# Kernel tuning notes

Measured on AMD Instinct MI355X. Metric: run time of the kernel, lower is better.

The kernel has to match this reference:

```python
import jax, jax.numpy as jnp
import numpy as np

EPS = 1e-8
SQRT_EPS_LOSS = 1e-6


def setup_inputs() -> dict:
    key = jax.random.key(0)
    ks = jax.random.split(key, 8)
    n_vars, n_clauses, n_edges, n_graphs = 500_000, 2_000_000, 6_000_000, 256
    dim, k = 128, 8
    x = jax.random.normal(ks[0], (n_vars, dim), jnp.float32)
    polarity = jnp.where(jax.random.bernoulli(ks[1], 0.5, (n_edges,)), 1.0, -1.0).astype(jnp.float32)
    variable_indices = jax.random.randint(ks[2], (n_edges,), 0, n_vars)
    clause_indices = jax.random.randint(ks[3], (n_edges,), 0, n_clauses)
    clause_batch = jnp.sort(jax.random.randint(ks[4], (n_clauses,), 0, n_graphs))
    W1 = jax.random.normal(ks[5], (dim, dim), jnp.float32) / np.sqrt(dim).astype(np.float32)
    b1 = jnp.zeros((dim,), jnp.float32)
    W2 = jax.random.normal(ks[6], (dim, k), jnp.float32) / np.sqrt(dim).astype(np.float32)
    b2 = jnp.zeros((k,), jnp.float32)
    return dict(x=x, polarity=polarity, variable_indices=variable_indices,
                clause_indices=clause_indices, clause_batch=clause_batch,
                W1=W1, b1=b1, W2=W2, b2=b2, n_graphs=n_graphs)


def reference(x, polarity, variable_indices, clause_indices, clause_batch, W1, b1, W2, b2, n_graphs):
    n_clauses = clause_batch.shape[0]
    k = W2.shape[1]

    # variables_output MLP: Linear -> ReLU -> Linear, [n_vars, k]
    logits = jax.nn.relu(x @ W1 + b1) @ W2 + b2

    # softplus_mixed_loss: gather literals along edges, scatter-sum into clauses
    lit = logits[variable_indices] * polarity[:, None]                      # [E, k]
    clause_sum = jax.ops.segment_sum(jax.nn.softplus(lit), clause_indices,
                                     num_segments=n_clauses)                # [C, k]
    clause_val = jnp.exp(-clause_sum)
    per_clause_loss = clause_val * (-jnp.log(1.0 - clause_val + EPS))       # [C, k]

    # per-graph soft loss
    per_graph_loss = jax.ops.segment_sum(per_clause_loss, clause_batch,
                                         num_segments=n_graphs)             # [G, k]
    per_graph_loss = jnp.sqrt(per_graph_loss + SQRT_EPS_LOSS) - np.float32(np.sqrt(SQRT_EPS_LOSS))

    costs = jnp.square(jnp.arange(1, k + 1, dtype=jnp.float32))             # [k]
    sorted_desc = -jnp.sort(-per_graph_loss, axis=-1)                       # descending sort per graph
    logit_loss = jnp.sum(sorted_desc * costs) / jnp.sum(costs)              # scalar

    # hard assignment check
    logits_hard = jnp.where(logits > 0, 1.0, -1.0)
    edge_hard = logits_hard[variable_indices] * polarity[:, None]           # [E, k]
    clauses_hard = jax.ops.segment_max(edge_hard, clause_indices,
                                       num_segments=n_clauses)              # amax per clause
    graphs_hard = jax.ops.segment_min(clauses_hard, clause_batch,
                                      num_segments=n_graphs)                # amin per graph
    solved = jnp.any(graphs_hard > 0.5, axis=1)                             # [G] bool

    return logit_loss, solved
```

## Files before the change

kernel.cpp:

```cpp
#include <hip/hip_runtime.h>
#include <hip/hip_bf16.h>

#define DIM 128
#define K 8
#define EPS 1e-8f
#define SQRT_EPS 1e-6f

#define CB 512
#define CSHIFT 9
#define NBMAX 4096
#define MAXSLOT 32
#define SARR_CAP 2560

#define TV1 8192
#define NT1MAX 1024
#define NKV 512
#define VSH 10
#define TB 4096
#define MAXTV 4
#define NKC 64
#define TC 4096
#define MAXTC 32

typedef __attribute__((ext_vector_type(8))) short bf16x8;
typedef __attribute__((ext_vector_type(4))) float f32x4;

__device__ inline short bfc(float f) {
    union { __hip_bfloat16 h; short s; } u;
    u.h = __float2bfloat16(f);
    return u.s;
}

#define LDW 136

__global__ __launch_bounds__(256) void mlp_kernel(
    const float* __restrict__ x, const float* __restrict__ W1,
    const float* __restrict__ b1, const float* __restrict__ W2,
    const float* __restrict__ b2, uint2* __restrict__ lfp8, int n_vars)
{
    __shared__ __align__(16) short w1t[DIM][LDW];
    __shared__ __align__(16) short w2t[16][LDW];
    __shared__ __align__(16) short hlds[4][16][LDW];
    __shared__ __align__(16) float lout[4][32][8];

    const int t = threadIdx.x;
    const int wave = t >> 6, lane = t & 63;
    const int lr = lane & 15, lg = lane >> 4;

    for (int i = t; i < DIM * DIM; i += 256) {
        int r = i >> 7, c = i & 127;
        w1t[c][r] = bfc(W1[i]);
    }
    for (int i = t; i < 16 * DIM; i += 256) {
        int c = i >> 7, j = i & 127;
        w2t[c][j] = (c < 8) ? bfc(W2[j * 8 + c]) : (short)0;
    }
    __syncthreads();

    const int rbase = blockIdx.x * 128 + wave * 32;

    bf16x8 a[2][4];
    #pragma unroll
    for (int rt = 0; rt < 2; ++rt) {
        int row = rbase + rt * 16 + lr;
        bool ok = row < n_vars;
        const float* xp = x + (size_t)row * DIM + lg * 8;
        #pragma unroll
        for (int kt = 0; kt < 4; ++kt) {
            bf16x8 av = {0,0,0,0,0,0,0,0};
            if (ok) {
                float4 f0 = *(const float4*)(xp + kt * 32);
                float4 f1 = *(const float4*)(xp + kt * 32 + 4);
                av[0]=bfc(f0.x); av[1]=bfc(f0.y); av[2]=bfc(f0.z); av[3]=bfc(f0.w);
                av[4]=bfc(f1.x); av[5]=bfc(f1.y); av[6]=bfc(f1.z); av[7]=bfc(f1.w);
            }
            a[rt][kt] = av;
        }
    }

    bf16x8 bb[4];
    #pragma unroll
    for (int kt = 0; kt < 4; ++kt)
        bb[kt] = *(const bf16x8*)&w2t[lr][kt * 32 + lg * 8];
    float b2v = (lr < 8) ? b2[lr] : 0.f;

    #pragma unroll
    for (int rt = 0; rt < 2; ++rt) {
        #pragma unroll
        for (int n = 0; n < 8; ++n) {
            f32x4 acc = {0.f, 0.f, 0.f, 0.f};
            #pragma unroll
            for (int kt = 0; kt < 4; ++kt) {
                bf16x8 bf = *(const bf16x8*)&w1t[n * 16 + lr][kt * 32 + lg * 8];
                acc = __builtin_amdgcn_mfma_f32_16x16x32_bf16(a[rt][kt], bf, acc, 0, 0, 0);
            }
            float bcol = b1[n * 16 + lr];
            #pragma unroll
            for (int r = 0; r < 4; ++r) {
                float h = fmaxf(acc[r] + bcol, 0.f);
                hlds[wave][lg * 4 + r][n * 16 + lr] = bfc(h);
            }
        }
        f32x4 acc2 = {0.f, 0.f, 0.f, 0.f};
        #pragma unroll
        for (int kt = 0; kt < 4; ++kt) {
            bf16x8 af = *(const bf16x8*)&hlds[wave][lr][kt * 32 + lg * 8];
            acc2 = __builtin_amdgcn_mfma_f32_16x16x32_bf16(af, bb[kt], acc2, 0, 0, 0);
        }
        if (lr < 8) {
            #pragma unroll
            for (int r = 0; r < 4; ++r)
                lout[wave][rt * 16 + lg * 4 + r][lr] = acc2[r] + b2v;
        }
    }

    __syncthreads();
    if (lane < 32) {
        int row = rbase + lane;
        if (row < n_vars) {
            const float* f = lout[wave][lane];
            unsigned lo = 0u, hi = 0u;
            lo = __builtin_amdgcn_cvt_pk_fp8_f32(f[0], f[1], lo, false);
            lo = __builtin_amdgcn_cvt_pk_fp8_f32(f[2], f[3], lo, true);
            hi = __builtin_amdgcn_cvt_pk_fp8_f32(f[4], f[5], hi, false);
            hi = __builtin_amdgcn_cvt_pk_fp8_f32(f[6], f[7], hi, true);
            lfp8[row] = make_uint2(lo, hi);
        }
    }
}


__global__ __launch_bounds__(256) void histV_kernel(
    const int* __restrict__ vi, unsigned* __restrict__ histV, int n_edges)
{
    __shared__ unsigned hl[NKV];
    const int t = threadIdx.x, b = blockIdx.x;
    for (int i = t; i < NKV; i += 256) hl[i] = 0u;
    __syncthreads();
    const int e0 = b * TV1, e1 = min(e0 + TV1, n_edges);
    for (int e = e0 + t; e < e1; e += 256)
        atomicAdd(&hl[((unsigned)vi[e]) >> VSH], 1u);
    __syncthreads();
    for (int i = t; i < NKV; i += 256) histV[(size_t)i * NT1MAX + b] = hl[i];
}

__global__ __launch_bounds__(256) void scanrowV_kernel(
    unsigned* __restrict__ hist, unsigned* __restrict__ btotal)
{
    const int t = threadIdx.x;
    const size_t base = (size_t)blockIdx.x * NT1MAX + t * 4;
    uint4 v = *(const uint4*)(hist + base);
    unsigned pre0 = 0, pre1 = v.x, pre2 = v.x + v.y, pre3 = v.x + v.y + v.z;
    unsigned run = pre3 + v.w;
    __shared__ unsigned ts[256];
    ts[t] = run;
    __syncthreads();
    for (int off = 1; off < 256; off <<= 1) {
        unsigned xv = (t >= off) ? ts[t - off] : 0u;
        __syncthreads();
        ts[t] += xv;
        __syncthreads();
    }
    unsigned ex = ts[t] - run;
    uint4 o = {ex + pre0, ex + pre1, ex + pre2, ex + pre3};
    *(uint4*)(hist + base) = o;
    if (t == 255) btotal[blockIdx.x] = ts[255];
}

__global__ void baseV_kernel(const unsigned* __restrict__ tv,
                             unsigned* __restrict__ bv)
{
    if (threadIdx.x == 0) {
        unsigned r = 0;
        for (int k = 0; k < NKV; ++k) { bv[k] = r; r += tv[k]; }
        bv[NKV] = r;
    }
}

__global__ __launch_bounds__(256) void scatterV_kernel(
    const int* __restrict__ ci, const int* __restrict__ vi,
    const float* __restrict__ pol, const unsigned* __restrict__ histV,
    const unsigned* __restrict__ baseV, unsigned* __restrict__ A, int n_edges)
{
    __shared__ unsigned sa[TV1];
    __shared__ unsigned short bmap[TV1];
    __shared__ unsigned h[NKV], lst[NKV], h2[NKV], gst[NKV];
    __shared__ unsigned ts[256];
    const int t = threadIdx.x, b = blockIdx.x;
    for (int i = t; i < NKV; i += 256) h[i] = 0u;
    __syncthreads();
    const int e0 = b * TV1, e1 = min(e0 + TV1, n_edges), n = e1 - e0;
    for (int e = e0 + t; e < e1; e += 256)
        atomicAdd(&h[((unsigned)vi[e]) >> VSH], 1u);
    __syncthreads();
    unsigned a0 = h[2 * t], a1 = h[2 * t + 1];
    unsigned run = a0 + a1;
    ts[t] = run;
    __syncthreads();
    for (int off = 1; off < 256; off <<= 1) {
        unsigned xv = (t >= off) ? ts[t - off] : 0u;
        __syncthreads();
        ts[t] += xv;
        __syncthreads();
    }
    unsigned ex = ts[t] - run;
    lst[2 * t] = ex; lst[2 * t + 1] = ex + a0;
    h2[2 * t] = ex;  h2[2 * t + 1] = ex + a0;
    __syncthreads();
    for (int e = e0 + t; e < e1; e += 256) {
        unsigned c = (unsigned)ci[e];
        unsigned v = (unsigned)vi[e];
        unsigned neg = (pol[e] < 0.f) ? 1u : 0u;
        unsigned k = v >> VSH;
        unsigned p = atomicAdd(&h2[k], 1u);
        sa[p] = c | (neg << 21) | ((v & ((1u << VSH) - 1u)) << 22);
        bmap[p] = (unsigned short)k;
    }
    for (int i = t; i < NKV; i += 256)
        gst[i] = baseV[i] + histV[(size_t)i * NT1MAX + b];
    __syncthreads();
    for (int s = t; s < n; s += 256) {
        unsigned k = bmap[s];
        A[gst[k] + (s - lst[k])] = sa[s];
    }
}


__global__ __launch_bounds__(256) void histB_kernel(
    const unsigned* __restrict__ A, const unsigned* __restrict__ baseV,
    unsigned* __restrict__ histB)
{
    __shared__ unsigned h[NKC];
    const int t = threadIdx.x;
    const int vg = blockIdx.x / MAXTV, i = blockIdx.x % MAXTV;
    const unsigned slo = baseV[vg], shi = baseV[vg + 1];
    const unsigned t0 = slo + (unsigned)i * TB;
    if (t0 >= shi) return;
    const unsigned t1 = min(t0 + TB, shi);
    if (t < NKC) h[t] = 0u;
    __syncthreads();
    for (unsigned e = t0 + t; e < t1; e += 256)
        atomicAdd(&h[(A[e] & 0x1FFFFFu) >> 15], 1u);
    __syncthreads();
    if (t < NKC) histB[(size_t)t * (NKV * MAXTV) + blockIdx.x] = h[t];
}

__global__ __launch_bounds__(256) void scanrowB_kernel(
    unsigned* __restrict__ hist, unsigned* __restrict__ btotal)
{
    const int t = threadIdx.x;
    const size_t base = (size_t)blockIdx.x * (NKV * MAXTV) + t * 8;
    uint4 v0 = *(const uint4*)(hist + base);
    uint4 v1 = *(const uint4*)(hist + base + 4);
    unsigned p0 = 0, p1 = v0.x, p2 = p1 + v0.y, p3 = p2 + v0.z, p4 = p3 + v0.w;
    unsigned p5 = p4 + v1.x, p6 = p5 + v1.y, p7 = p6 + v1.z;
    unsigned run = p7 + v1.w;
    __shared__ unsigned ts[256];
    ts[t] = run;
    __syncthreads();
    for (int off = 1; off < 256; off <<= 1) {
        unsigned xv = (t >= off) ? ts[t - off] : 0u;
        __syncthreads();
        ts[t] += xv;
        __syncthreads();
    }
    unsigned ex = ts[t] - run;
    uint4 o0 = {ex + p0, ex + p1, ex + p2, ex + p3};
    uint4 o1 = {ex + p4, ex + p5, ex + p6, ex + p7};
    *(uint4*)(hist + base) = o0;
    *(uint4*)(hist + base + 4) = o1;
    if (t == 255) btotal[blockIdx.x] = ts[255];
}

__global__ void baseB_kernel(const unsigned* __restrict__ tb,
                             unsigned* __restrict__ bb)
{
    if (threadIdx.x == 0) {
        unsigned r = 0;
        for (int k = 0; k < NKC; ++k) { bb[k] = r; r += tb[k]; }
        bb[NKC] = r;
    }
}

__global__ __launch_bounds__(256) void scatterB_kernel(
    const unsigned* __restrict__ A, const uint2* __restrict__ lfp8,
    const unsigned* __restrict__ baseV, const unsigned* __restrict__ histB,
    const unsigned* __restrict__ baseB, unsigned short* __restrict__ B1,
    uint2* __restrict__ B2, int n_vars)
{
    __shared__ uint2 slice[1 << VSH];
    __shared__ unsigned short st1[TB];
    __shared__ uint2 st2[TB];
    __shared__ unsigned char bmap[TB];
    __shared__ unsigned h[NKC], lst[NKC], h2[NKC], gst[NKC];
    const int t = threadIdx.x;
    const int vg = blockIdx.x / MAXTV, i = blockIdx.x % MAXTV;
    const unsigned slo = baseV[vg], shi = baseV[vg + 1];
    const unsigned t0 = slo + (unsigned)i * TB;
    if (t0 >= shi) return;
    const unsigned t1 = min(t0 + TB, shi);
    const int n = (int)(t1 - t0);
    for (int s = t; s < (1 << VSH); s += 256) {
        int v = (vg << VSH) + s;
        slice[s] = (v < n_vars) ? lfp8[v] : make_uint2(0u, 0u);
    }
    if (t < NKC) h[t] = 0u;
    __syncthreads();
    for (unsigned e = t0 + t; e < t1; e += 256)
        atomicAdd(&h[(A[e] & 0x1FFFFFu) >> 15], 1u);
    __syncthreads();
    if (t == 0) {
        unsigned r = 0;
        for (int k = 0; k < NKC; ++k) { lst[k] = r; h2[k] = r; r += h[k]; }
    }
    __syncthreads();
    for (unsigned e = t0 + t; e < t1; e += 256) {
        unsigned a = A[e];
        unsigned c = a & 0x1FFFFFu;
        unsigned k = c >> 15;
        unsigned p = atomicAdd(&h2[k], 1u);
        uint2 g = slice[a >> 22];
        unsigned sm = ((a >> 21) & 1u) * 0x80808080u;
        g.x ^= sm; g.y ^= sm;
        st1[p] = (unsigned short)(c & 0x7FFFu);
        st2[p] = g;
        bmap[p] = (unsigned char)k;
    }
    if (t < NKC) gst[t] = baseB[t] + histB[(size_t)t * (NKV * MAXTV) + blockIdx.x];
    __syncthreads();
    for (int s = t; s < n; s += 256) {
        unsigned k = bmap[s];
        unsigned pos = gst[k] + (s - lst[k]);
        B1[pos] = st1[s];
        B2[pos] = st2[s];
    }
}


__global__ __launch_bounds__(256) void histC_kernel(
    const unsigned short* __restrict__ B1, const unsigned* __restrict__ baseB,
    unsigned* __restrict__ histC)
{
    __shared__ unsigned h[64];
    const int t = threadIdx.x;
    const int k1 = blockIdx.x / MAXTC, i = blockIdx.x % MAXTC;
    const unsigned slo = baseB[k1], shi = baseB[k1 + 1];
    const unsigned t0 = slo + (unsigned)i * TC;
    if (t0 >= shi) return;
    const unsigned t1 = min(t0 + TC, shi);
    if (t < 64) h[t] = 0u;
    __syncthreads();
    for (unsigned e = t0 + t; e < t1; e += 256)
        atomicAdd(&h[((unsigned)B1[e] >> 9) & 63u], 1u);
    __syncthreads();
    if (t < 64) histC[(size_t)(k1 * 64 + t) * MAXTC + i] = h[t];
}

__global__ __launch_bounds__(256) void scanrowC_kernel(
    unsigned* __restrict__ histC, unsigned* __restrict__ ctotal)
{
    const int rid = blockIdx.x * 256 + threadIdx.x;
    unsigned r = 0;
    for (int i = 0; i < MAXTC; ++i) {
        unsigned v = histC[(size_t)rid * MAXTC + i];
        histC[(size_t)rid * MAXTC + i] = r;
        r += v;
    }
    ctotal[rid] = r;
}

__global__ __launch_bounds__(256) void bbase_kernel(
    const unsigned* __restrict__ ctotal, unsigned* __restrict__ bbase, int nb)
{
    const int t = threadIdx.x;
    unsigned loc[16];
    unsigned run = 0;
    #pragma unroll
    for (int it = 0; it < 16; ++it) {
        int idx = t * 16 + it;
        unsigned v = (idx < 4096) ? ctotal[idx] : 0u;
        loc[it] = run;
        run += v;
    }
    __shared__ unsigned ts[256];
    ts[t] = run;
    __syncthreads();
    for (int off = 1; off < 256; off <<= 1) {
        unsigned xv = (t >= off) ? ts[t - off] : 0u;
        __syncthreads();
        ts[t] += xv;
        __syncthreads();
    }
    unsigned ex = ts[t] - run;
    #pragma unroll
    for (int it = 0; it < 16; ++it) {
        int idx = t * 16 + it;
        if (idx <= nb) bbase[idx] = ex + loc[it];
    }
}

__global__ __launch_bounds__(256) void scatterC_kernel(
    const unsigned short* __restrict__ B1, const uint2* __restrict__ B2,
    const unsigned* __restrict__ baseB, const unsigned* __restrict__ histC,
    const unsigned* __restrict__ bbase, unsigned short* __restrict__ sortedS,
    uint2* __restrict__ sortedL)
{
    __shared__ unsigned short st1[TC];
    __shared__ uint2 st2[TC];
    __shared__ unsigned char bmap[TC];
    __shared__ unsigned h[64], lst[64], h2[64], gst[64];
    const int t = threadIdx.x;
    const int k1 = blockIdx.x / MAXTC, i = blockIdx.x % MAXTC;
    const unsigned slo = baseB[k1], shi = baseB[k1 + 1];
    const unsigned t0 = slo + (unsigned)i * TC;
    if (t0 >= shi) return;
    const unsigned t1 = min(t0 + TC, shi);
    const int n = (int)(t1 - t0);
    if (t < 64) h[t] = 0u;
    __syncthreads();
    for (unsigned e = t0 + t; e < t1; e += 256)
        atomicAdd(&h[((unsigned)B1[e] >> 9) & 63u], 1u);
    __syncthreads();
    if (t == 0) {
        unsigned r = 0;
        for (int k = 0; k < 64; ++k) { lst[k] = r; h2[k] = r; r += h[k]; }
    }
    __syncthreads();
    for (unsigned e = t0 + t; e < t1; e += 256) {
        unsigned b = (unsigned)B1[e];
        unsigned k2 = (b >> 9) & 63u;
        unsigned p = atomicAdd(&h2[k2], 1u);
        st1[p] = (unsigned short)(b & 0x1FFu);
        st2[p] = B2[e];
        bmap[p] = (unsigned char)k2;
    }
    if (t < 64) {
        unsigned cbk = (unsigned)(k1 * 64 + t);
        gst[t] = bbase[cbk] + histC[(size_t)cbk * MAXTC + i];
    }
    __syncthreads();
    for (int s = t; s < n; s += 256) {
        unsigned k = bmap[s];
        unsigned pos = gst[k] + (s - lst[k]);
        sortedS[pos] = st1[s];
        sortedL[pos] = st2[s];
    }
}

__global__ __launch_bounds__(256) void bucket_kernel(
    const unsigned short* __restrict__ sortedS, const uint2* __restrict__ sortedL,
    const unsigned* __restrict__ bbase, const int* __restrict__ clause_batch,
    float* __restrict__ per_graph, unsigned* __restrict__ gmask,
    int n_clauses, int n_graphs)
{
    __shared__ uint2 sarrL[SARR_CAP];
    __shared__ unsigned cnt[CB];
    __shared__ unsigned cofs[CB];
    __shared__ unsigned cst[CB + 1];
    __shared__ unsigned cmsk[CB];
    __shared__ float pcl[CB * K];
    __shared__ float sp[256];
    __shared__ float pg[MAXSLOT * K];
    __shared__ unsigned pmask[MAXSLOT];
    __shared__ unsigned ts[256];
    __shared__ int sh_ghi;

    const int t = threadIdx.x;
    const int bkt = blockIdx.x;
    const int c_base = bkt << CSHIFT;
    const int n_cl = min(CB, n_clauses - c_base);
    const int g_lo = clause_batch[c_base];

    {
        float v = __builtin_amdgcn_cvt_f32_fp8((unsigned)t, 0);
        sp[t] = fmaxf(v, 0.f) + __logf(1.f + __expf(-fabsf(v)));
    }
    for (int i = t; i < CB; i += 256) cnt[i] = 0u;
    for (int i = t; i < MAXSLOT * K; i += 256) pg[i] = 0.f;
    if (t < MAXSLOT) pmask[t] = 0xFFu;
    if (t == 0) sh_ghi = clause_batch[c_base + n_cl - 1];
    __syncthreads();

    const unsigned lo = bbase[bkt], hi = bbase[bkt + 1];
    const int ne = (int)(hi - lo);

    if (ne <= SARR_CAP) {
        for (unsigned e = lo + t; e < hi; e += 256)
            atomicAdd(&cnt[sortedS[e] & 511u], 1u);
        __syncthreads();
        unsigned a0 = cnt[2 * t], a1 = cnt[2 * t + 1];
        unsigned run = a0 + a1;
        ts[t] = run;
        __syncthreads();
        for (int off = 1; off < 256; off <<= 1) {
            unsigned xv = (t >= off) ? ts[t - off] : 0u;
            __syncthreads();
            ts[t] += xv;
            __syncthreads();
        }
        unsigned ex = ts[t] - run;
        cst[2 * t] = ex; cst[2 * t + 1] = ex + a0;
        cofs[2 * t] = ex; cofs[2 * t + 1] = ex + a0;
        if (t == 255) cst[CB] = ex + run;
        __syncthreads();
        for (unsigned e = lo + t; e < hi; e += 256) {
            unsigned cl = sortedS[e] & 511u;
            unsigned p = atomicAdd(&cofs[cl], 1u);
            sarrL[p] = sortedL[e];
        }
        __syncthreads();
        #pragma unroll
        for (int oc = 0; oc < 2; ++oc) {
            int cl = 2 * t + oc;
            if (cl >= n_cl) continue;
            unsigned s0 = cst[cl];
            int n = (int)(cst[cl + 1] - s0);
            float sums[K] = {0.f, 0.f, 0.f, 0.f, 0.f, 0.f, 0.f, 0.f};
            unsigned ormask = 0u;
            for (int base = 0; base < n; base += 8) {
                int m = min(8, n - base);
                uint2 gs[8];
                for (int i2 = 0; i2 < m; ++i2) gs[i2] = sarrL[s0 + base + i2];
                for (int i2 = 0; i2 < m; ++i2) {
                    #pragma unroll
                    for (int j = 0; j < 4; ++j) {
                        unsigned b0 = (gs[i2].x >> (8 * j)) & 0xFFu;
                        unsigned b1 = (gs[i2].y >> (8 * j)) & 0xFFu;
                        sums[j]     += sp[b0];
                        sums[j + 4] += sp[b1];
                        ormask |= (b0 - 1u < 0x7Fu) ? (1u << j) : 0u;
                        ormask |= (b1 - 1u < 0x7Fu) ? (1u << (j + 4)) : 0u;
                    }
                }
            }
            #pragma unroll
            for (int j = 0; j < K; ++j) {
                float cv = __expf(-sums[j]);
                pcl[cl * K + j] = cv * (-__logf(1.f - cv + EPS));
            }
            cmsk[cl] = ormask;
        }
    } else {
        for (int i = t; i < CB * K; i += 256) pcl[i] = 0.f;
        for (int i = t; i < CB; i += 256) cmsk[i] = 0u;
        __syncthreads();
        for (unsigned e = lo + t; e < hi; e += 256) {
            unsigned cl = sortedS[e] & 511u;
            uint2 g = sortedL[e];
            unsigned gt0 = 0u;
            #pragma unroll
            for (int j = 0; j < 4; ++j) {
                unsigned b0 = (g.x >> (8 * j)) & 0xFFu;
                unsigned b1 = (g.y >> (8 * j)) & 0xFFu;
                atomicAdd(&pcl[cl * K + j], sp[b0]);
                atomicAdd(&pcl[cl * K + j + 4], sp[b1]);
                gt0 |= (b0 - 1u < 0x7Fu) ? (1u << j) : 0u;
                gt0 |= (b1 - 1u < 0x7Fu) ? (1u << (j + 4)) : 0u;
            }
            atomicOr(&cmsk[cl], gt0);
        }
        __syncthreads();
        for (int oc = 0; oc < 2; ++oc) {
            int cl = 2 * t + oc;
            if (cl >= n_cl) continue;
            #pragma unroll
            for (int j = 0; j < K; ++j) {
                float cv = __expf(-pcl[cl * K + j]);
                pcl[cl * K + j] = cv * (-__logf(1.f - cv + EPS));
            }
        }
    }
    __syncthreads();

    float lacc[K];
    unsigned land = 0xFFu;
    int cur = -1;
    for (int cl = t; cl < n_cl; cl += 256) {
        int gg = clause_batch[c_base + cl];
        int slot = gg - g_lo;
        if (slot != cur) {
            if (cur >= 0) {
                if (cur < MAXSLOT) {
                    #pragma unroll
                    for (int j = 0; j < K; ++j) atomicAdd(&pg[cur * K + j], lacc[j]);
                    atomicAnd(&pmask[cur], land);
                } else {
                    #pragma unroll
                    for (int j = 0; j < K; ++j) atomicAdd(&per_graph[(size_t)(g_lo + cur) * K + j], lacc[j]);
                    atomicAnd(&gmask[g_lo + cur], land);
                }
            }
            cur = slot;
            #pragma unroll
            for (int j = 0; j < K; ++j) lacc[j] = 0.f;
            land = 0xFFu;
        }
        land &= cmsk[cl];
        #pragma unroll
        for (int j = 0; j < K; ++j) lacc[j] += pcl[cl * K + j];
    }
    if (cur >= 0) {
        if (cur < MAXSLOT) {
            #pragma unroll
            for (int j = 0; j < K; ++j) atomicAdd(&pg[cur * K + j], lacc[j]);
            atomicAnd(&pmask[cur], land);
        } else {
            #pragma unroll
            for (int j = 0; j < K; ++j) atomicAdd(&per_graph[(size_t)(g_lo + cur) * K + j], lacc[j]);
            atomicAnd(&gmask[g_lo + cur], land);
        }
    }
    __syncthreads();

    const int nslots = min(sh_ghi - g_lo + 1, MAXSLOT);
    if (t < nslots * K) {
        int s = t >> 3, j = t & 7;
        atomicAdd(&per_graph[(size_t)(g_lo + s) * K + j], pg[s * K + j]);
    }
    if (t < nslots) atomicAnd(&gmask[g_lo + t], pmask[t]);
}

__global__ __launch_bounds__(256) void final_kernel(
    const float* __restrict__ per_graph, const unsigned* __restrict__ gmask,
    int n_graphs, float* __restrict__ out)
{
    const int t = threadIdx.x;
    float dot = 0.f;
    if (t < n_graphs) {
        float v[K];
        #pragma unroll
        for (int j = 0; j < K; ++j)
            v[j] = sqrtf(per_graph[(size_t)t * K + j] + SQRT_EPS) - sqrtf(SQRT_EPS);
        #pragma unroll
        for (int i = 1; i < K; ++i) {
            float key = v[i];
            int j = i - 1;
            while (j >= 0 && v[j] < key) { v[j + 1] = v[j]; --j; }
            v[j + 1] = key;
        }
        #pragma unroll
        for (int i = 0; i < K; ++i)
            dot = fmaf(v[i], (float)((i + 1) * (i + 1)), dot);
        out[1 + t] = (gmask[t] & 0xFFu) ? 1.f : 0.f;
    }
    __shared__ float red[256];
    red[t] = dot;
    __syncthreads();
    for (int s = 128; s >= 1; s >>= 1) {
        if (t < s) red[t] += red[t + s];
        __syncthreads();
    }
    if (t == 0) out[0] = red[0] * (1.f / 204.f);
}

extern "C" void kernel_launch(void* const* d_in, const int* in_sizes, int n_in,
                              void* d_out, int out_size, void* d_ws, size_t ws_size,
                              hipStream_t stream) {
    const float* x   = (const float*)d_in[0];
    const float* pol = (const float*)d_in[1];
    const int* vi    = (const int*)d_in[2];
    const int* ci    = (const int*)d_in[3];
    const int* cb    = (const int*)d_in[4];
    const float* W1  = (const float*)d_in[5];
    const float* b1  = (const float*)d_in[6];
    const float* W2  = (const float*)d_in[7];
    const float* b2  = (const float*)d_in[8];

    const int n_vars    = in_sizes[0] / DIM;
    const int n_edges   = in_sizes[1];
    const int n_clauses = in_sizes[4];
    const int n_graphs  = out_size - 1;
    const int nb        = (n_clauses + CB - 1) / CB;
    const int nt1       = (n_edges + TV1 - 1) / TV1;

    char* ws = (char*)d_ws;
    size_t off = 0;
    auto alloc = [&](size_t bytes) { char* p = ws + off; off += (bytes + 255) & ~(size_t)255; return p; };
    uint2*    lfp8   = (uint2*)alloc((size_t)n_vars * 8);
    unsigned* A      = (unsigned*)alloc((size_t)n_edges * 4);
    unsigned short* B1 = (unsigned short*)alloc((size_t)n_edges * 2);
    uint2*    B2     = (uint2*)alloc((size_t)n_edges * 8);
    uint2*    sortedL= (uint2*)alloc((size_t)n_edges * 8);
    unsigned* histV  = (unsigned*)alloc((size_t)NKV * NT1MAX * 4);
    unsigned* histB  = (unsigned*)alloc((size_t)NKC * NKV * MAXTV * 4);
    unsigned* histC  = (unsigned*)alloc((size_t)4096 * MAXTC * 4);
    unsigned* btotalV= (unsigned*)alloc((size_t)(NKV + 1) * 4);
    unsigned* baseV  = (unsigned*)alloc((size_t)(NKV + 1) * 4);
    unsigned* btotalB= (unsigned*)alloc((size_t)(NKC + 1) * 4);
    unsigned* baseB  = (unsigned*)alloc((size_t)(NKC + 1) * 4);
    unsigned* ctotal = (unsigned*)alloc((size_t)4096 * 4);
    unsigned* bbase  = (unsigned*)alloc((size_t)(NBMAX + 1) * 4);
    float*    per_graph = (float*)alloc((size_t)n_graphs * K * 4);
    unsigned* gmask  = (unsigned*)alloc((size_t)n_graphs * 4);
    unsigned short* sortedS = (unsigned short*)A;

    hipMemsetAsync(histV, 0, (size_t)NKV * NT1MAX * 4, stream);
    hipMemsetAsync(histB, 0, (size_t)NKC * NKV * MAXTV * 4, stream);
    hipMemsetAsync(histC, 0, (size_t)4096 * MAXTC * 4, stream);
    hipMemsetAsync(per_graph, 0, (size_t)n_graphs * K * 4, stream);
    hipMemsetAsync(gmask, 0xFF, (size_t)n_graphs * 4, stream);

    mlp_kernel<<<(n_vars + 127) / 128, 256, 0, stream>>>(x, W1, b1, W2, b2, lfp8, n_vars);

    histV_kernel<<<nt1, 256, 0, stream>>>(vi, histV, n_edges);
    scanrowV_kernel<<<NKV, 256, 0, stream>>>(histV, btotalV);
    baseV_kernel<<<1, 64, 0, stream>>>(btotalV, baseV);
    scatterV_kernel<<<nt1, 256, 0, stream>>>(ci, vi, pol, histV, baseV, A, n_edges);

    histB_kernel<<<NKV * MAXTV, 256, 0, stream>>>(A, baseV, histB);
    scanrowB_kernel<<<NKC, 256, 0, stream>>>(histB, btotalB);
    baseB_kernel<<<1, 64, 0, stream>>>(btotalB, baseB);
    scatterB_kernel<<<NKV * MAXTV, 256, 0, stream>>>(A, lfp8, baseV, histB, baseB,
                                                     B1, B2, n_vars);

    histC_kernel<<<NKC * MAXTC, 256, 0, stream>>>(B1, baseB, histC);
    scanrowC_kernel<<<16, 256, 0, stream>>>(histC, ctotal);
    bbase_kernel<<<1, 256, 0, stream>>>(ctotal, bbase, nb);
    scatterC_kernel<<<NKC * MAXTC, 256, 0, stream>>>(B1, B2, baseB, histC, bbase,
                                                     sortedS, sortedL);

    bucket_kernel<<<nb, 256, 0, stream>>>(sortedS, sortedL, bbase, cb,
                                          per_graph, gmask, n_clauses, n_graphs);
    final_kernel<<<1, 256, 0, stream>>>(per_graph, gmask, n_graphs, (float*)d_out);
}
```

Before: 510.0 us.

## Shrink bucket kernel LDS with wave-shuffle scan and register-held clause losses

Replaces the block-wide shared-memory Hillis-Steele prefix scan with a wavefront shuffle scan plus a 4-entry cross-wave combine, removing many __syncthreads. Per-clause losses and masks are now kept in registers instead of the pcl/cmsk shared arrays, and the fallback path reuses sarrL/cnt as scratch. Each thread directly atomically adds its two clauses into per-graph slots, merging them when they share a graph. This reduces LDS footprint (pcl was 16KB), which may raise occupancy, but the per-thread atomics replace the strided accumulation loop, increasing shared atomic contention on pg.

```diff
diff --git a/kernel.cpp b/kernel.cpp
--- a/kernel.cpp
+++ b/kernel.cpp
@@ -455,17 +455,15 @@
 {
     __shared__ uint2 sarrL[SARR_CAP];
     __shared__ unsigned cnt[CB];
-    __shared__ unsigned cofs[CB];
     __shared__ unsigned cst[CB + 1];
-    __shared__ unsigned cmsk[CB];
-    __shared__ float pcl[CB * K];
     __shared__ float sp[256];
     __shared__ float pg[MAXSLOT * K];
     __shared__ unsigned pmask[MAXSLOT];
-    __shared__ unsigned ts[256];
+    __shared__ unsigned wtot[4];
     __shared__ int sh_ghi;
 
     const int t = threadIdx.x;
+    const int lane = t & 63, wv = t >> 6;
     const int bkt = blockIdx.x;
     const int c_base = bkt << CSHIFT;
     const int n_cl = min(CB, n_clauses - c_base);
@@ -484,28 +482,35 @@
     const unsigned lo = bbase[bkt], hi = bbase[bkt + 1];
     const int ne = (int)(hi - lo);
 
+    float loss0[K], loss1[K];
+    unsigned msk0 = 0u, msk1 = 0u;
+    bool have0 = false, have1 = false;
+
     if (ne <= SARR_CAP) {
         for (unsigned e = lo + t; e < hi; e += 256)
             atomicAdd(&cnt[sortedS[e] & 511u], 1u);
         __syncthreads();
         unsigned a0 = cnt[2 * t], a1 = cnt[2 * t + 1];
         unsigned run = a0 + a1;
-        ts[t] = run;
-        __syncthreads();
-        for (int off = 1; off < 256; off <<= 1) {
-            unsigned xv = (t >= off) ? ts[t - off] : 0u;
-            __syncthreads();
-            ts[t] += xv;
-            __syncthreads();
-        }
-        unsigned ex = ts[t] - run;
+        unsigned incl = run;
+        #pragma unroll
+        for (int off = 1; off < 64; off <<= 1) {
+            unsigned v = __shfl_up(incl, off, 64);
+            if (lane >= off) incl += v;
+        }
+        if (lane == 63) wtot[wv] = incl;
+        __syncthreads();
+        unsigned wpre = 0;
+        #pragma unroll
+        for (int w = 0; w < 3; ++w) if (w < wv) wpre += wtot[w];
+        unsigned ex = wpre + incl - run;
         cst[2 * t] = ex; cst[2 * t + 1] = ex + a0;
-        cofs[2 * t] = ex; cofs[2 * t + 1] = ex + a0;
+        cnt[2 * t] = ex; cnt[2 * t + 1] = ex + a0;
         if (t == 255) cst[CB] = ex + run;
         __syncthreads();
         for (unsigned e = lo + t; e < hi; e += 256) {
             unsigned cl = sortedS[e] & 511u;
-            unsigned p = atomicAdd(&cofs[cl], 1u);
+            unsigned p = atomicAdd(&cnt[cl], 1u);
             sarrL[p] = sortedL[e];
         }
         __syncthreads();
@@ -533,16 +538,20 @@
                     }
                 }
             }
+            float* lss = oc ? loss1 : loss0;
             #pragma unroll
             for (int j = 0; j < K; ++j) {
                 float cv = __expf(-sums[j]);
-                pcl[cl * K + j] = cv * (-__logf(1.f - cv + EPS));
+                lss[j] = cv * (-__logf(1.f - cv + EPS));
             }
-            cmsk[cl] = ormask;
+            if (oc) { msk1 = ormask; have1 = true; }
+            else    { msk0 = ormask; have0 = true; }
         }
     } else {
-        for (int i = t; i < CB * K; i += 256) pcl[i] = 0.f;
-        for (int i = t; i < CB; i += 256) cmsk[i] = 0u;
+        float* acc = (float*)sarrL;
+        unsigned* fmsk = cnt;
+        for (int i = t; i < CB * K; i += 256) acc[i] = 0.f;
+        for (int i = t; i < CB; i += 256) fmsk[i] = 0u;
         __syncthreads();
         for (unsigned e = lo + t; e < hi; e += 256) {
             unsigned cl = sortedS[e] & 511u;
@@ -552,62 +561,57 @@
             for (int j = 0; j < 4; ++j) {
                 unsigned b0 = (g.x >> (8 * j)) & 0xFFu;
                 unsigned b1 = (g.y >> (8 * j)) & 0xFFu;
-                atomicAdd(&pcl[cl * K + j], sp[b0]);
-                atomicAdd(&pcl[cl * K + j + 4], sp[b1]);
+                atomicAdd(&acc[cl * K + j], sp[b0]);
+                atomicAdd(&acc[cl * K + j + 4], sp[b1]);
                 gt0 |= (b0 - 1u < 0x7Fu) ? (1u << j) : 0u;
                 gt0 |= (b1 - 1u < 0x7Fu) ? (1u << (j + 4)) : 0u;
             }
-            atomicOr(&cmsk[cl], gt0);
-        }
-        __syncthreads();
+            atomicOr(&fmsk[cl], gt0);
+        }
+        __syncthreads();
+        #pragma unroll
         for (int oc = 0; oc < 2; ++oc) {
             int cl = 2 * t + oc;
             if (cl >= n_cl) continue;
+            float* lss = oc ? loss1 : loss0;
             #pragma unroll
             for (int j = 0; j < K; ++j) {
-                float cv = __expf(-pcl[cl * K + j]);
-                pcl[cl * K + j] = cv * (-__logf(1.f - cv + EPS));
+                float cv = __expf(-acc[cl * K + j]);
+                lss[j] = cv * (-__logf(1.f - cv + EPS));
             }
-        }
-    }
-    __syncthreads();
-
-    float lacc[K];
-    unsigned land = 0xFFu;
-    int cur = -1;
-    for (int cl = t; cl < n_cl; cl += 256) {
-        int gg = clause_batch[c_base + cl];
-        int slot = gg - g_lo;
-        if (slot != cur) {
-            if (cur >= 0) {
-                if (cur < MAXSLOT) {
-                    #pragma unroll
-                    for (int j = 0; j < K; ++j) atomicAdd(&pg[cur * K + j], lacc[j]);
-                    atomicAnd(&pmask[cur], land);
-                } else {
-                    #pragma unroll
-                    for (int j = 0; j < K; ++j) atomicAdd(&per_graph[(size_t)(g_lo + cur) * K + j], lacc[j]);
-                    atomicAnd(&gmask[g_lo + cur], land);
-                }
+            if (oc) { msk1 = fmsk[cl]; have1 = true; }
+            else    { msk0 = fmsk[cl]; have0 = true; }
+        }
+    }
+
+    if (have0) {
+        int slot0 = clause_batch[c_base + 2 * t] - g_lo;
+        int slot1 = have1 ? (clause_batch[c_base + 2 * t + 1] - g_lo) : -1;
+        if (have1 && slot1 == slot0) {
+            #pragma unroll
+            for (int j = 0; j < K; ++j) loss0[j] += loss1[j];
+            msk0 &= msk1;
+            have1 = false;
+        }
+        if (slot0 < MAXSLOT) {
+            #pragma unroll
+            for (int j = 0; j < K; ++j) atomicAdd(&pg[slot0 * K + j], loss0[j]);
+            atomicAnd(&pmask[slot0], msk0);
+        } else {
+            #pragma unroll
+            for (int j = 0; j < K; ++j) atomicAdd(&per_graph[(size_t)(g_lo + slot0) * K + j], loss0[j]);
+            atomicAnd(&gmask[g_lo + slot0], msk0);
+        }
+        if (have1) {
+            if (slot1 < MAXSLOT) {
+                #pragma unroll
+                for (int j = 0; j < K; ++j) atomicAdd(&pg[slot1 * K + j], loss1[j]);
+                atomicAnd(&pmask[slot1], msk1);
+            } else {
+                #pragma unroll
+                for (int j = 0; j < K; ++j) atomicAdd(&per_graph[(size_t)(g_lo + slot1) * K + j], loss1[j]);
+                atomicAnd(&gmask[g_lo + slot1], msk1);
             }
-            cur = slot;
-            #pragma unroll
-            for (int j = 0; j < K; ++j) lacc[j] = 0.f;
-            land = 0xFFu;
-        }
-        land &= cmsk[cl];
-        #pragma unroll
-        for (int j = 0; j < K; ++j) lacc[j] += pcl[cl * K + j];
-    }
-    if (cur >= 0) {
-        if (cur < MAXSLOT) {
-            #pragma unroll
-            for (int j = 0; j < K; ++j) atomicAdd(&pg[cur * K + j], lacc[j]);
-            atomicAnd(&pmask[cur], land);
-        } else {
-            #pragma unroll
-            for (int j = 0; j < K; ++j) atomicAdd(&per_graph[(size_t)(g_lo + cur) * K + j], lacc[j]);
-            atomicAnd(&gmask[g_lo + cur], land);
         }
     }
     __syncthreads();
```

Result: faster. 474.8 us (-6.9%).
